# Kernel tuning notes

Hardware: AMD Instinct MI355X
Metric: run time of the kernel (lower is better)

## Reference

```python
import jax, jax.numpy as jnp
import numpy as np

N_NODES = 100000
N_EDGES = 1600000
IN_CH = 128
OUT_CH = 64
HID = 2 * OUT_CH


def setup_inputs() -> dict:
    key = jax.random.key(0)
    ks = jax.random.split(key, 9)
    x = jax.random.normal(ks[0], (N_NODES, IN_CH), dtype=jnp.float32)
    edge_index = jax.random.randint(ks[1], (2, N_EDGES), 0, N_NODES, dtype=jnp.int64)
    s = 0.05
    W1 = jax.random.normal(ks[2], (IN_CH, HID), dtype=jnp.float32) * s
    b1 = jnp.zeros((HID,), dtype=jnp.float32)
    Wmu = jax.random.normal(ks[3], (HID, OUT_CH), dtype=jnp.float32) * s
    bmu = jnp.zeros((OUT_CH,), dtype=jnp.float32)
    Wls = jax.random.normal(ks[4], (HID, OUT_CH), dtype=jnp.float32) * s
    bls = jnp.zeros((OUT_CH,), dtype=jnp.float32)
    eps = jax.random.normal(ks[5], (N_NODES, OUT_CH), dtype=jnp.float32)
    return {"x": x, "edge_index": edge_index, "W1": W1, "b1": b1,
            "Wmu": Wmu, "bmu": bmu, "Wls": Wls, "bls": bls, "eps": eps}


def _gcn_conv(x, W, b, src, dst, dis):
    # PyG GCNConv: out = D^{-1/2}(A+I)D^{-1/2} X W + b, self-loops added.
    h = x @ W  # [N, F]
    norm = dis[src] * dis[dst]  # per-edge symmetric norm
    msg = h[src] * norm[:, None]  # [E, F] gathered + scaled messages
    agg = jax.ops.segment_sum(msg, dst, num_segments=x.shape[0])
    agg = agg + h * (dis * dis)[:, None]  # self-loop term
    return agg + b


def reference(x, edge_index, W1, b1, Wmu, bmu, Wls, bls, eps):
    src, dst = edge_index[0], edge_index[1]
    N = x.shape[0]
    # degree over A + I (aggregation at dst, +1 for self loop)
    deg = jax.ops.segment_sum(jnp.ones_like(dst, dtype=x.dtype), dst,
                              num_segments=N) + 1.0
    dis = jax.lax.rsqrt(deg)  # deg >= 1, safe
    h = _gcn_conv(x, W1, b1, src, dst, dis)
    mu = _gcn_conv(h, Wmu, bmu, src, dst, dis)
    logstd = _gcn_conv(h, Wls, bls, src, dst, dis)
    z = mu + eps * jnp.exp(logstd)  # reparametrization trick
    return (z, mu, logstd)
```

## Files before the change

### kernel.cpp

```cpp
#include <hip/hip_runtime.h>
#include <hip/hip_bf16.h>


typedef unsigned int u32;
typedef unsigned short u16;
typedef unsigned char u8;
typedef __bf16 bf16x8 __attribute__((ext_vector_type(8)));
typedef float f32x4 __attribute__((ext_vector_type(4)));
typedef int i32x4 __attribute__((ext_vector_type(4)));

__device__ __forceinline__ u16 f2bf(float f) {
    union { float f; u32 u; } v; v.f = f;
    u32 u = v.u;
    u += 0x7fffu + ((u >> 16) & 1u);
    return (u16)(u >> 16);
}
__device__ __forceinline__ float bflo(u32 p) {
    union { u32 u; float f; } v; v.u = p << 16; return v.f;
}
__device__ __forceinline__ float bfhi(u32 p) {
    union { u32 u; float f; } v; v.u = p & 0xffff0000u; return v.f;
}

__global__ __launch_bounds__(256) void deg_hist(const int* __restrict__ dst,
                                                u32* __restrict__ deg,
                                                u8* __restrict__ loc, int E) {
    int i4 = (blockIdx.x * 256 + threadIdx.x) * 4;
    if (i4 + 3 < E) {
        i32x4 d4 = __builtin_nontemporal_load((const i32x4*)(dst + i4));
        u32 l0 = atomicAdd(&deg[d4.x], 1u) & 0xffu;
        u32 l1 = atomicAdd(&deg[d4.y], 1u) & 0xffu;
        u32 l2 = atomicAdd(&deg[d4.z], 1u) & 0xffu;
        u32 l3 = atomicAdd(&deg[d4.w], 1u) & 0xffu;
        u32 packed = l0 | (l1 << 8) | (l2 << 16) | (l3 << 24);
        __builtin_nontemporal_store(packed, (u32*)(loc + i4));
    } else {
        for (int i = i4; i < E; ++i) loc[i] = (u8)atomicAdd(&deg[dst[i]], 1u);
    }
}

__global__ __launch_bounds__(256) void scanA(const u32* __restrict__ deg,
                                             u32* __restrict__ blockSums, int N) {
    __shared__ u32 s[256];
    int t = threadIdx.x, i = blockIdx.x * 256 + t;
    s[t] = (i < N) ? deg[i] : 0u;
    for (int off = 128; off > 0; off >>= 1) {
        __syncthreads();
        if (t < off) s[t] += s[t + off];
    }
    if (t == 0) blockSums[blockIdx.x] = s[0];
}

__global__ __launch_bounds__(512) void scanB(const u32* __restrict__ blockSums,
                                             u32* __restrict__ blockOffs, int NB) {
    __shared__ u32 s[512];
    int t = threadIdx.x;
    u32 v = (t < NB) ? blockSums[t] : 0u;
    s[t] = v;
    for (int off = 1; off < 512; off <<= 1) {
        __syncthreads();
        u32 add = (t >= off) ? s[t - off] : 0u;
        __syncthreads();
        s[t] += add;
    }
    __syncthreads();
    if (t < NB) blockOffs[t] = s[t] - v;
}

__global__ __launch_bounds__(256) void scanC(const u32* __restrict__ deg,
                                             const u32* __restrict__ blockOffs,
                                             u32* __restrict__ rowstart,
                                             float* __restrict__ dis, int N, int E) {
    __shared__ u32 s[256];
    int t = threadIdx.x, i = blockIdx.x * 256 + t;
    u32 v = (i < N) ? deg[i] : 0u;
    s[t] = v;
    for (int off = 1; off < 256; off <<= 1) {
        __syncthreads();
        u32 add = (t >= off) ? s[t - off] : 0u;
        __syncthreads();
        s[t] += add;
    }
    __syncthreads();
    if (i < N) {
        rowstart[i] = blockOffs[blockIdx.x] + s[t] - v;
        dis[i] = rsqrtf((float)v + 1.0f);
    }
    if (i == 0) rowstart[N] = (u32)E;
}

__global__ __launch_bounds__(256) void place_kernel(const int* __restrict__ src,
                                                    const int* __restrict__ dst,
                                                    const u8* __restrict__ loc,
                                                    const u32* __restrict__ rowstart,
                                                    int* __restrict__ csr, int E) {
    int i4 = (blockIdx.x * 256 + threadIdx.x) * 4;
    if (i4 + 3 < E) {
        i32x4 s4 = __builtin_nontemporal_load((const i32x4*)(src + i4));
        i32x4 d4 = __builtin_nontemporal_load((const i32x4*)(dst + i4));
        u32 l4 = __builtin_nontemporal_load((const u32*)(loc + i4));
        csr[rowstart[d4.x] + (l4 & 0xffu)] = s4.x;
        csr[rowstart[d4.y] + ((l4 >> 8) & 0xffu)] = s4.y;
        csr[rowstart[d4.z] + ((l4 >> 16) & 0xffu)] = s4.z;
        csr[rowstart[d4.w] + (l4 >> 24)] = s4.w;
    } else {
        for (int i = i4; i < E; ++i) csr[rowstart[dst[i]] + loc[i]] = src[i];
    }
}

__global__ __launch_bounds__(256) void fuse_w(const float* __restrict__ W1,
                                              const float* __restrict__ Wmu,
                                              const float* __restrict__ Wls,
                                              const float* __restrict__ b1,
                                              const float* __restrict__ bmu,
                                              const float* __restrict__ bls,
                                              u16* __restrict__ WfT,
                                              float* __restrict__ bb,
                                              float* __restrict__ bcat) {
    int idx = blockIdx.x * 256 + threadIdx.x;
    if (idx >= 16384) return;
    int k = idx >> 7, n = idx & 127;
    const float* Wcol = (n < 64) ? (Wmu + n) : (Wls + (n - 64));
    float acc = 0.f;
#pragma unroll 8
    for (int j = 0; j < 128; ++j) acc += W1[k * 128 + j] * Wcol[j * 64];
    WfT[n * 128 + k] = f2bf(acc);
    if (k == 0) {
        float accb = 0.f;
#pragma unroll 8
        for (int j = 0; j < 128; ++j) accb += b1[j] * Wcol[j * 64];
        bb[n] = accb;
        bcat[n] = (n < 64) ? bmu[n] : bls[n - 64];
    }
}

__global__ __launch_bounds__(256) void convert_x(const float* __restrict__ x,
                                                 const float* __restrict__ dis,
                                                 u32* __restrict__ xs,
                                                 u32* __restrict__ ts, int N) {
    long i = (long)blockIdx.x * 256 + threadIdx.x;
    long node = i >> 5;
    if (node > N) return;
    if (node == N) {
        ((uint2*)xs)[i] = make_uint2(0u, 0u);
        ((uint2*)ts)[i] = make_uint2(0u, 0u);
        return;
    }
    float dd = dis[node];
    f32x4 v = ((const f32x4*)x)[i];
    u32 p0 = (u32)f2bf(v[0] * dd) | ((u32)f2bf(v[1] * dd) << 16);
    u32 p1 = (u32)f2bf(v[2] * dd) | ((u32)f2bf(v[3] * dd) << 16);
    ((uint2*)xs)[i] = make_uint2(p0, p1);
}

__global__ __launch_bounds__(256) void g1gemm(const u32* __restrict__ xs,
                                              const int* __restrict__ csr,
                                              const u32* __restrict__ rowstart,
                                              const float* __restrict__ dis,
                                              const u16* __restrict__ WfT,
                                              const float* __restrict__ bb,
                                              u16* __restrict__ ts, int N) {
    __shared__ __align__(16) u16 ytile[16][136];
    __shared__ float disS[16];
    int tid = threadIdx.x, blk = blockIdx.x;
    int wave = tid >> 6, lane = tid & 63;
    int sub = lane >> 4, l = lane & 15;
    int nl = wave * 4 + sub;
    int node = blk * 16 + nl;
    bool live = node < N;
    int nodeC = live ? node : 0;
    float dd = dis[nodeC];
    u32 beg = live ? rowstart[nodeC] : 0u;
    u32 end = live ? rowstart[nodeC + 1] : 0u;
    if (tid < 16) disS[tid] = (blk * 16 + tid < N) ? dis[blk * 16 + tid] : 0.f;

    const uint4* xs4 = (const uint4*)xs;
    uint4 selfv = xs4[(long)nodeC * 16 + l];
    float a0 = bflo(selfv.x), a1 = bfhi(selfv.x);
    float a2 = bflo(selfv.y), a3 = bfhi(selfv.y);
    float a4 = bflo(selfv.z), a5 = bfhi(selfv.z);
    float a6 = bflo(selfv.w), a7 = bfhi(selfv.w);

    int s = (beg + (u32)l < end) ? csr[beg + l] : N;
    for (u32 e0 = beg; e0 < end; e0 += 16) {
        u32 e1 = e0 + 16;
        int sn = (e1 < end && e1 + (u32)l < end) ? csr[e1 + l] : N;
        uint4 w[16];
#pragma unroll
        for (int j = 0; j < 16; ++j) {
            int sj = __shfl(s, sub * 16 + j);
            w[j] = xs4[(long)sj * 16 + l];
        }
#pragma unroll
        for (int j = 0; j < 16; ++j) {
            a0 += bflo(w[j].x); a1 += bfhi(w[j].x);
            a2 += bflo(w[j].y); a3 += bfhi(w[j].y);
            a4 += bflo(w[j].z); a5 += bfhi(w[j].z);
            a6 += bflo(w[j].w); a7 += bfhi(w[j].w);
        }
        s = sn;
    }
    uint4 o = make_uint4(0u, 0u, 0u, 0u);
    if (live) {
        o.x = (u32)f2bf(a0 * dd) | ((u32)f2bf(a1 * dd) << 16);
        o.y = (u32)f2bf(a2 * dd) | ((u32)f2bf(a3 * dd) << 16);
        o.z = (u32)f2bf(a4 * dd) | ((u32)f2bf(a5 * dd) << 16);
        o.w = (u32)f2bf(a6 * dd) | ((u32)f2bf(a7 * dd) << 16);
    }
    *(uint4*)&ytile[nl][l * 8] = o;
    __syncthreads();

    int quad = sub, mn = l;
    bf16x8 af[4];
#pragma unroll
    for (int kk = 0; kk < 4; ++kk)
        af[kk] = *reinterpret_cast<const bf16x8*>(&ytile[mn][kk * 32 + quad * 8]);

#pragma unroll
    for (int n0 = 0; n0 < 2; ++n0) {
        int col = wave * 32 + n0 * 16 + mn;
        f32x4 acc = {0.f, 0.f, 0.f, 0.f};
#pragma unroll
        for (int kk = 0; kk < 4; ++kk) {
            bf16x8 bf =
                *reinterpret_cast<const bf16x8*>(&WfT[col * 128 + kk * 32 + quad * 8]);
            acc = __builtin_amdgcn_mfma_f32_16x16x32_bf16(af[kk], bf, acc, 0, 0, 0);
        }
        float bc = bb[col];
#pragma unroll
        for (int r = 0; r < 4; ++r) {
            int row = quad * 4 + r;
            int gn = blk * 16 + row;
            if (gn < N)
                __builtin_nontemporal_store(f2bf((acc[r] + bc) * disS[row]),
                                            ts + (long)gn * 128 + col);
        }
    }
}

__global__ __launch_bounds__(256) void gather2(const u32* __restrict__ ts,
                                               const int* __restrict__ csr,
                                               const u32* __restrict__ rowstart,
                                               const float* __restrict__ dis,
                                               const float* __restrict__ bcat,
                                               const float* __restrict__ eps,
                                               float* __restrict__ out, int N) {
    int wid = (blockIdx.x * 256 + threadIdx.x) >> 6;
    int sub = (threadIdx.x & 63) >> 4, l = threadIdx.x & 15;
    int node = wid * 4 + sub;
    bool live = node < N;
    int nodeC = live ? node : 0;
    float dd = dis[nodeC];
    u32 beg = live ? rowstart[nodeC] : 0u;
    u32 end = live ? rowstart[nodeC + 1] : 0u;
    const uint4* ts4 = (const uint4*)ts;

    uint4 selfv = ts4[(long)nodeC * 16 + l];
    float a0 = bflo(selfv.x), a1 = bfhi(selfv.x);
    float a2 = bflo(selfv.y), a3 = bfhi(selfv.y);
    float a4 = bflo(selfv.z), a5 = bfhi(selfv.z);
    float a6 = bflo(selfv.w), a7 = bfhi(selfv.w);

    int s = (beg + (u32)l < end) ? csr[beg + l] : N;
    for (u32 e0 = beg; e0 < end; e0 += 16) {
        u32 e1 = e0 + 16;
        int sn = (e1 < end && e1 + (u32)l < end) ? csr[e1 + l] : N;
        uint4 w[16];
#pragma unroll
        for (int j = 0; j < 16; ++j) {
            int sj = __shfl(s, sub * 16 + j);
            w[j] = ts4[(long)sj * 16 + l];
        }
#pragma unroll
        for (int j = 0; j < 16; ++j) {
            a0 += bflo(w[j].x); a1 += bfhi(w[j].x);
            a2 += bflo(w[j].y); a3 += bfhi(w[j].y);
            a4 += bflo(w[j].z); a5 += bfhi(w[j].z);
            a6 += bflo(w[j].w); a7 += bfhi(w[j].w);
        }
        s = sn;
    }

    int c0 = l * 8;
    f32x4 clo = ((const f32x4*)bcat)[2 * l], chi = ((const f32x4*)bcat)[2 * l + 1];
    float v0 = a0 * dd + clo[0];
    float v1 = a1 * dd + clo[1];
    float v2 = a2 * dd + clo[2];
    float v3 = a3 * dd + clo[3];
    float v4 = a4 * dd + chi[0];
    float v5 = a5 * dd + chi[1];
    float v6 = a6 * dd + chi[2];
    float v7 = a7 * dd + chi[3];

    int srcl = (threadIdx.x & 63) + 8;
    float w0 = __shfl(v0, srcl), w1 = __shfl(v1, srcl), w2 = __shfl(v2, srcl),
          w3 = __shfl(v3, srcl), w4 = __shfl(v4, srcl), w5 = __shfl(v5, srcl),
          w6 = __shfl(v6, srcl), w7 = __shfl(v7, srcl);

    if (!live) return;
    long NO = (long)N * 64;
    if (l < 8) {
        float* mu = out + NO + (long)node * 64 + c0;
        __builtin_nontemporal_store(f32x4{v0, v1, v2, v3}, (f32x4*)mu);
        __builtin_nontemporal_store(f32x4{v4, v5, v6, v7}, (f32x4*)mu + 1);
        const f32x4* ep = (const f32x4*)(eps + (long)node * 64 + c0);
        f32x4 e0v = __builtin_nontemporal_load(ep);
        f32x4 e1v = __builtin_nontemporal_load(ep + 1);
        float* z = out + (long)node * 64 + c0;
        f32x4 z0 = {v0 + e0v[0] * __expf(w0), v1 + e0v[1] * __expf(w1),
                    v2 + e0v[2] * __expf(w2), v3 + e0v[3] * __expf(w3)};
        f32x4 z1 = {v4 + e1v[0] * __expf(w4), v5 + e1v[1] * __expf(w5),
                    v6 + e1v[2] * __expf(w6), v7 + e1v[3] * __expf(w7)};
        __builtin_nontemporal_store(z0, (f32x4*)z);
        __builtin_nontemporal_store(z1, (f32x4*)z + 1);
    } else {
        float* ls = out + 2 * NO + (long)node * 64 + (c0 - 64);
        __builtin_nontemporal_store(f32x4{v0, v1, v2, v3}, (f32x4*)ls);
        __builtin_nontemporal_store(f32x4{v4, v5, v6, v7}, (f32x4*)ls + 1);
    }
}

extern "C" void kernel_launch(void* const* d_in, const int* in_sizes, int n_in,
                              void* d_out, int out_size, void* d_ws, size_t ws_size,
                              hipStream_t stream) {
    const float* x   = (const float*)d_in[0];
    const int* ei    = (const int*)d_in[1];
    const float* W1  = (const float*)d_in[2];
    const float* b1  = (const float*)d_in[3];
    const float* Wmu = (const float*)d_in[4];
    const float* bmu = (const float*)d_in[5];
    const float* Wls = (const float*)d_in[6];
    const float* bls = (const float*)d_in[7];
    const float* eps = (const float*)d_in[8];
    float* out = (float*)d_out;

    const int N = in_sizes[0] / 128;
    const int E = in_sizes[1] / 2;
    const int* src = ei;
    const int* dst = ei + E;
    const int NB = (N + 255) / 256;

    char* ws = (char*)d_ws;
    u32* deg       = (u32*)(ws + 0);
    u32* rowstart  = (u32*)(ws + 401408);
    u32* blockSums = (u32*)(ws + 802816);
    u32* blockOffs = (u32*)(ws + 804864);
    float* dis     = (float*)(ws + 806912);
    u16* WfT       = (u16*)(ws + 1208320);
    float* bb      = (float*)(ws + 1241088);
    float* bcat    = (float*)(ws + 1241600);
    u8* loc        = (u8*)(ws + 1242112);
    int* csr       = (int*)(ws + 2842112);
    u32* xs        = (u32*)(ws + 9242112);
    u32* ts        = (u32*)(ws + 34842368);

    hipMemsetAsync(deg, 0, 400000, stream);

    int gridE4 = (E / 4 + 255) / 256;
    deg_hist<<<gridE4, 256, 0, stream>>>(dst, deg, loc, E);
    scanA<<<NB, 256, 0, stream>>>(deg, blockSums, N);
    scanB<<<1, 512, 0, stream>>>(blockSums, blockOffs, NB);
    scanC<<<NB, 256, 0, stream>>>(deg, blockOffs, rowstart, dis, N, E);
    place_kernel<<<gridE4, 256, 0, stream>>>(src, dst, loc, rowstart, csr, E);
    fuse_w<<<64, 256, 0, stream>>>(W1, Wmu, Wls, b1, bmu, bls, WfT, bb, bcat);

    long Qc = (long)(N + 1) * 32;
    convert_x<<<(int)((Qc + 255) / 256), 256, 0, stream>>>(x, dis, xs, ts, N);

    int gridT = (N + 15) / 16;
    g1gemm<<<gridT, 256, 0, stream>>>(xs, csr, rowstart, dis, WfT, bb,
                                      (u16*)ts, N);

    int gridG = ((N + 3) / 4 * 64 + 255) / 256;
    gather2<<<gridG, 256, 0, stream>>>(ts, csr, rowstart, dis, bcat, eps, out, N);
}
```

Before: 421.7 us.

## Split each node's edge list across two half-groups in both gather kernels

Both the first-layer aggregation and the second gather now give each node 32 lanes instead of 16. The two 16-lane halves each process half of the edge list in chunks of 8 and then combine their partial sums with a cross-half shuffle. g1gemm moves to 512-thread blocks so one block still covers 16 nodes, and each wave's MFMA stage now produces one 16-column tile instead of two. The aim is more memory-level parallelism per node and shorter serial loops, at the price of twice as many threads, idle lanes in the index loads, and half of the lanes doing nothing during the epilogue.

```diff
diff --git a/kernel.cpp b/kernel.cpp
--- a/kernel.cpp
+++ b/kernel.cpp
@@ -153,7 +153,7 @@
     ((uint2*)xs)[i] = make_uint2(p0, p1);
 }
 
-__global__ __launch_bounds__(256) void g1gemm(const u32* __restrict__ xs,
+__global__ __launch_bounds__(512) void g1gemm(const u32* __restrict__ xs,
                                               const int* __restrict__ csr,
                                               const u32* __restrict__ rowstart,
                                               const float* __restrict__ dis,
@@ -164,35 +164,42 @@
     __shared__ float disS[16];
     int tid = threadIdx.x, blk = blockIdx.x;
     int wave = tid >> 6, lane = tid & 63;
-    int sub = lane >> 4, l = lane & 15;
-    int nl = wave * 4 + sub;
+    int nsub = lane >> 5;
+    int h = (lane >> 4) & 1;
+    int l = lane & 15;
+    int nl = wave * 2 + nsub;
     int node = blk * 16 + nl;
     bool live = node < N;
     int nodeC = live ? node : 0;
     float dd = dis[nodeC];
     u32 beg = live ? rowstart[nodeC] : 0u;
     u32 end = live ? rowstart[nodeC + 1] : 0u;
+    u32 cut = beg + ((end - beg + 1u) >> 1);
+    u32 mybeg = h ? cut : beg;
+    u32 myend = h ? end : cut;
     if (tid < 16) disS[tid] = (blk * 16 + tid < N) ? dis[blk * 16 + tid] : 0.f;
 
     const uint4* xs4 = (const uint4*)xs;
     uint4 selfv = xs4[(long)nodeC * 16 + l];
-    float a0 = bflo(selfv.x), a1 = bfhi(selfv.x);
-    float a2 = bflo(selfv.y), a3 = bfhi(selfv.y);
-    float a4 = bflo(selfv.z), a5 = bfhi(selfv.z);
-    float a6 = bflo(selfv.w), a7 = bfhi(selfv.w);
-
-    int s = (beg + (u32)l < end) ? csr[beg + l] : N;
-    for (u32 e0 = beg; e0 < end; e0 += 16) {
-        u32 e1 = e0 + 16;
-        int sn = (e1 < end && e1 + (u32)l < end) ? csr[e1 + l] : N;
-        uint4 w[16];
-#pragma unroll
-        for (int j = 0; j < 16; ++j) {
-            int sj = __shfl(s, sub * 16 + j);
+    bool h0 = (h == 0);
+    float a0 = h0 ? bflo(selfv.x) : 0.f, a1 = h0 ? bfhi(selfv.x) : 0.f;
+    float a2 = h0 ? bflo(selfv.y) : 0.f, a3 = h0 ? bfhi(selfv.y) : 0.f;
+    float a4 = h0 ? bflo(selfv.z) : 0.f, a5 = h0 ? bfhi(selfv.z) : 0.f;
+    float a6 = h0 ? bflo(selfv.w) : 0.f, a7 = h0 ? bfhi(selfv.w) : 0.f;
+
+    int sbase = nsub * 32 + h * 16;
+    int s = (l < 8 && mybeg + (u32)l < myend) ? csr[mybeg + l] : N;
+    for (u32 e0 = mybeg; e0 < myend; e0 += 8) {
+        u32 e1 = e0 + 8;
+        int sn = (l < 8 && e1 < myend && e1 + (u32)l < myend) ? csr[e1 + l] : N;
+        uint4 w[8];
+#pragma unroll
+        for (int j = 0; j < 8; ++j) {
+            int sj = __shfl(s, sbase + j);
             w[j] = xs4[(long)sj * 16 + l];
         }
 #pragma unroll
-        for (int j = 0; j < 16; ++j) {
+        for (int j = 0; j < 8; ++j) {
             a0 += bflo(w[j].x); a1 += bfhi(w[j].x);
             a2 += bflo(w[j].y); a3 += bfhi(w[j].y);
             a4 += bflo(w[j].z); a5 += bfhi(w[j].z);
@@ -200,6 +207,11 @@
         }
         s = sn;
     }
+    a0 += __shfl_xor(a0, 16); a1 += __shfl_xor(a1, 16);
+    a2 += __shfl_xor(a2, 16); a3 += __shfl_xor(a3, 16);
+    a4 += __shfl_xor(a4, 16); a5 += __shfl_xor(a5, 16);
+    a6 += __shfl_xor(a6, 16); a7 += __shfl_xor(a7, 16);
+
     uint4 o = make_uint4(0u, 0u, 0u, 0u);
     if (live) {
         o.x = (u32)f2bf(a0 * dd) | ((u32)f2bf(a1 * dd) << 16);
@@ -207,34 +219,31 @@
         o.z = (u32)f2bf(a4 * dd) | ((u32)f2bf(a5 * dd) << 16);
         o.w = (u32)f2bf(a6 * dd) | ((u32)f2bf(a7 * dd) << 16);
     }
-    *(uint4*)&ytile[nl][l * 8] = o;
+    if (h0) *(uint4*)&ytile[nl][l * 8] = o;
     __syncthreads();
 
-    int quad = sub, mn = l;
+    int quad = lane >> 4, mn = l;
     bf16x8 af[4];
 #pragma unroll
     for (int kk = 0; kk < 4; ++kk)
         af[kk] = *reinterpret_cast<const bf16x8*>(&ytile[mn][kk * 32 + quad * 8]);
 
-#pragma unroll
-    for (int n0 = 0; n0 < 2; ++n0) {
-        int col = wave * 32 + n0 * 16 + mn;
-        f32x4 acc = {0.f, 0.f, 0.f, 0.f};
-#pragma unroll
-        for (int kk = 0; kk < 4; ++kk) {
-            bf16x8 bf =
-                *reinterpret_cast<const bf16x8*>(&WfT[col * 128 + kk * 32 + quad * 8]);
-            acc = __builtin_amdgcn_mfma_f32_16x16x32_bf16(af[kk], bf, acc, 0, 0, 0);
-        }
-        float bc = bb[col];
-#pragma unroll
-        for (int r = 0; r < 4; ++r) {
-            int row = quad * 4 + r;
-            int gn = blk * 16 + row;
-            if (gn < N)
-                __builtin_nontemporal_store(f2bf((acc[r] + bc) * disS[row]),
-                                            ts + (long)gn * 128 + col);
-        }
+    int col = wave * 16 + mn;
+    f32x4 acc = {0.f, 0.f, 0.f, 0.f};
+#pragma unroll
+    for (int kk = 0; kk < 4; ++kk) {
+        bf16x8 bf =
+            *reinterpret_cast<const bf16x8*>(&WfT[col * 128 + kk * 32 + quad * 8]);
+        acc = __builtin_amdgcn_mfma_f32_16x16x32_bf16(af[kk], bf, acc, 0, 0, 0);
+    }
+    float bc = bb[col];
+#pragma unroll
+    for (int r = 0; r < 4; ++r) {
+        int row = quad * 4 + r;
+        int gn = blk * 16 + row;
+        if (gn < N)
+            __builtin_nontemporal_store(f2bf((acc[r] + bc) * disS[row]),
+                                        ts + (long)gn * 128 + col);
     }
 }
 
@@ -245,34 +254,41 @@
                                                const float* __restrict__ bcat,
                                                const float* __restrict__ eps,
                                                float* __restrict__ out, int N) {
-    int wid = (blockIdx.x * 256 + threadIdx.x) >> 6;
-    int sub = (threadIdx.x & 63) >> 4, l = threadIdx.x & 15;
-    int node = wid * 4 + sub;
+    int tid = threadIdx.x;
+    int gw = (blockIdx.x * 256 + tid) >> 6;
+    int lane = tid & 63;
+    int nsub = lane >> 5, h = (lane >> 4) & 1, l = lane & 15;
+    int node = gw * 2 + nsub;
     bool live = node < N;
     int nodeC = live ? node : 0;
     float dd = dis[nodeC];
     u32 beg = live ? rowstart[nodeC] : 0u;
     u32 end = live ? rowstart[nodeC + 1] : 0u;
+    u32 cut = beg + ((end - beg + 1u) >> 1);
+    u32 mybeg = h ? cut : beg;
+    u32 myend = h ? end : cut;
     const uint4* ts4 = (const uint4*)ts;
 
     uint4 selfv = ts4[(long)nodeC * 16 + l];
-    float a0 = bflo(selfv.x), a1 = bfhi(selfv.x);
-    float a2 = bflo(selfv.y), a3 = bfhi(selfv.y);
-    float a4 = bflo(selfv.z), a5 = bfhi(selfv.z);
-    float a6 = bflo(selfv.w), a7 = bfhi(selfv.w);
-
-    int s = (beg + (u32)l < end) ? csr[beg + l] : N;
-    for (u32 e0 = beg; e0 < end; e0 += 16) {
-        u32 e1 = e0 + 16;
-        int sn = (e1 < end && e1 + (u32)l < end) ? csr[e1 + l] : N;
-        uint4 w[16];
-#pragma unroll
-        for (int j = 0; j < 16; ++j) {
-            int sj = __shfl(s, sub * 16 + j);
+    bool h0 = (h == 0);
+    float a0 = h0 ? bflo(selfv.x) : 0.f, a1 = h0 ? bfhi(selfv.x) : 0.f;
+    float a2 = h0 ? bflo(selfv.y) : 0.f, a3 = h0 ? bfhi(selfv.y) : 0.f;
+    float a4 = h0 ? bflo(selfv.z) : 0.f, a5 = h0 ? bfhi(selfv.z) : 0.f;
+    float a6 = h0 ? bflo(selfv.w) : 0.f, a7 = h0 ? bfhi(selfv.w) : 0.f;
+
+    int sbase = nsub * 32 + h * 16;
+    int s = (l < 8 && mybeg + (u32)l < myend) ? csr[mybeg + l] : N;
+    for (u32 e0 = mybeg; e0 < myend; e0 += 8) {
+        u32 e1 = e0 + 8;
+        int sn = (l < 8 && e1 < myend && e1 + (u32)l < myend) ? csr[e1 + l] : N;
+        uint4 w[8];
+#pragma unroll
+        for (int j = 0; j < 8; ++j) {
+            int sj = __shfl(s, sbase + j);
             w[j] = ts4[(long)sj * 16 + l];
         }
 #pragma unroll
-        for (int j = 0; j < 16; ++j) {
+        for (int j = 0; j < 8; ++j) {
             a0 += bflo(w[j].x); a1 += bfhi(w[j].x);
             a2 += bflo(w[j].y); a3 += bfhi(w[j].y);
             a4 += bflo(w[j].z); a5 += bfhi(w[j].z);
@@ -280,6 +296,10 @@
         }
         s = sn;
     }
+    a0 += __shfl_xor(a0, 16); a1 += __shfl_xor(a1, 16);
+    a2 += __shfl_xor(a2, 16); a3 += __shfl_xor(a3, 16);
+    a4 += __shfl_xor(a4, 16); a5 += __shfl_xor(a5, 16);
+    a6 += __shfl_xor(a6, 16); a7 += __shfl_xor(a7, 16);
 
     int c0 = l * 8;
     f32x4 clo = ((const f32x4*)bcat)[2 * l], chi = ((const f32x4*)bcat)[2 * l + 1];
@@ -292,12 +312,12 @@
     float v6 = a6 * dd + chi[2];
     float v7 = a7 * dd + chi[3];
 
-    int srcl = (threadIdx.x & 63) + 8;
+    int srcl = lane + 8;
     float w0 = __shfl(v0, srcl), w1 = __shfl(v1, srcl), w2 = __shfl(v2, srcl),
           w3 = __shfl(v3, srcl), w4 = __shfl(v4, srcl), w5 = __shfl(v5, srcl),
           w6 = __shfl(v6, srcl), w7 = __shfl(v7, srcl);
 
-    if (!live) return;
+    if (!live || h != 0) return;
     long NO = (long)N * 64;
     if (l < 8) {
         float* mu = out + NO + (long)node * 64 + c0;
@@ -368,9 +388,9 @@
     convert_x<<<(int)((Qc + 255) / 256), 256, 0, stream>>>(x, dis, xs, ts, N);
 
     int gridT = (N + 15) / 16;
-    g1gemm<<<gridT, 256, 0, stream>>>(xs, csr, rowstart, dis, WfT, bb,
+    g1gemm<<<gridT, 512, 0, stream>>>(xs, csr, rowstart, dis, WfT, bb,
                                       (u16*)ts, N);
 
-    int gridG = ((N + 3) / 4 * 64 + 255) / 256;
+    int gridG = (((N + 1) / 2 + 3) / 4);
     gather2<<<gridG, 256, 0, stream>>>(ts, csr, rowstart, dis, bcat, eps, out, N);
 }
```

After: 411.3 us. 2.5% less time.
